# Optimization experiments

Measured on AMD Instinct MI355X. Metric: run time of the kernel, lower is better.

The kernel has to match this reference:

```python
import jax, jax.numpy as jnp
import numpy as np
import math

B, S, DIN, DQ, DV = 8, 2048, 1024, 1024, 1024


def setup_inputs() -> dict:
    key = jax.random.key(0)
    ks = jax.random.split(key, 9)
    c_q = math.sqrt(6.0 / (DIN + DQ))
    c_v = math.sqrt(6.0 / (DIN + DV))
    query = jax.random.normal(ks[0], (B, S, DIN), dtype=jnp.float32)
    key_t = jax.random.normal(ks[1], (B, S, DIN), dtype=jnp.float32)
    value = jax.random.normal(ks[2], (B, S, DIN), dtype=jnp.float32)
    # Linear weights stored as [in, out] for x @ W; uniform init per module
    Wq = jax.random.uniform(ks[3], (DIN, DQ), jnp.float32, -c_q, c_q)
    Wk = jax.random.uniform(ks[4], (DIN, DQ), jnp.float32, -c_q, c_q)
    Wv = jax.random.uniform(ks[5], (DIN, DV), jnp.float32, -c_v, c_v)
    bq = jax.random.uniform(ks[6], (DQ,), jnp.float32, -c_q, c_q)
    bk = jax.random.uniform(ks[7], (DQ,), jnp.float32, -c_q, c_q)
    bv = jax.random.uniform(ks[8], (DV,), jnp.float32, -c_v, c_v)
    # causal mask: True where attention is disallowed (masked_fill semantics)
    mask = jnp.broadcast_to(jnp.triu(jnp.ones((S, S), dtype=bool), k=1), (B, S, S))
    return {"query": query, "key": key_t, "value": value,
            "Wq": Wq, "bq": bq, "Wk": Wk, "bk": bk, "Wv": Wv, "bv": bv,
            "mask": mask}


def reference(query, key, value, Wq, bq, Wk, bk, Wv, bv, mask):
    q = query @ Wq + bq                       # [B,S,DQ]
    k = key @ Wk + bk                         # [B,S,DQ]
    v = value @ Wv + bv                       # [B,S,DV]
    scores = jnp.einsum('bsd,btd->bst', q, k) / math.sqrt(DQ)  # [B,S,S]
    scores = jnp.where(mask, jnp.float32(-1e9), scores)
    weights = jax.nn.softmax(scores, axis=2)
    y = jnp.einsum('bst,btd->bsd', weights, v)  # [B,S,DV]
    return y
```

## Files before the change

### kernel.cpp

```cpp
#include <hip/hip_runtime.h>


typedef unsigned short u16;
typedef unsigned int   u32;
typedef float f32x4 __attribute__((ext_vector_type(4)));
typedef short s16x8 __attribute__((ext_vector_type(8)));

__device__ __forceinline__ u16 f2bf(float x) {
  u32 u = __builtin_bit_cast(u32, x);
  u += 0x7fffu + ((u >> 16) & 1u);
  return (u16)(u >> 16);
}
__device__ __forceinline__ float bf2f(u16 h) {
  u32 u = (u32)h << 16;
  return __builtin_bit_cast(float, u);
}

__device__ __forceinline__ void gld_lds16(const u16* g, u16* l) {
  __builtin_amdgcn_global_load_lds((const __attribute__((address_space(1))) void*)g,
                                   (__attribute__((address_space(3))) void*)l,
                                   16, 0, 0);
}

__global__ __launch_bounds__(256) void cvt_bf16_3(const float* __restrict__ i0,
                                                  const float* __restrict__ i1,
                                                  const float* __restrict__ i2,
                                                  u16* __restrict__ out, long X) {
  const float* in = blockIdx.y == 0 ? i0 : (blockIdx.y == 1 ? i1 : i2);
  long i = (long)blockIdx.x * 256 + threadIdx.x;
  float4 v = ((const float4*)in)[i];
  ushort4 o;
  o.x = f2bf(v.x); o.y = f2bf(v.y); o.z = f2bf(v.z); o.w = f2bf(v.w);
  ((ushort4*)(out + blockIdx.y * X))[i] = o;
}

__global__ __launch_bounds__(256) void transpose_w3(const float* __restrict__ w0,
                                                    const float* __restrict__ w1,
                                                    const float* __restrict__ w2,
                                                    u16* __restrict__ Wt,
                                                    int K, int N, long WN) {
  __shared__ u16 t[32][33];
  const float* W = blockIdx.z == 0 ? w0 : (blockIdx.z == 1 ? w1 : w2);
  u16* out = Wt + blockIdx.z * WN;
  int n0 = blockIdx.x * 32, k0 = blockIdx.y * 32;
  int tx = threadIdx.x & 31, ty = threadIdx.x >> 5;
  for (int r = ty; r < 32; r += 8)
    t[r][tx] = f2bf(W[(long)(k0 + r) * N + n0 + tx]);
  __syncthreads();
  for (int r = ty; r < 32; r += 8)
    out[(long)(n0 + r) * K + k0 + tx] = t[tx][r];
}

__global__ __launch_bounds__(256) void transpose_v(const u16* __restrict__ v,
                                                   u16* __restrict__ vt,
                                                   int S, int D) {
  __shared__ u16 t[32][33];
  long b = blockIdx.z;
  const u16* vb = v + b * S * D;
  u16* vtb = vt + b * S * D;
  int d0 = blockIdx.x * 32, s0 = blockIdx.y * 32;
  int tx = threadIdx.x & 31, ty = threadIdx.x >> 5;
  for (int r = ty; r < 32; r += 8)
    t[r][tx] = vb[(long)(s0 + r) * D + d0 + tx];
  __syncthreads();
  for (int r = ty; r < 32; r += 8)
    vtb[(long)(d0 + r) * S + s0 + tx] = t[tx][r];
}

__device__ __forceinline__ void gemm_core(const u16* __restrict__ At,
                                          const u16* __restrict__ Bt,
                                          int lda, int ldb, int ktEnd,
                                          f32x4 (&acc)[4][4],
                                          u16* lA, u16* lB) {
  const int tid = threadIdx.x;
  const int lane = tid & 63, half = lane >> 4, l16 = lane & 15;
  const int wave = tid >> 6;
  const int wm = (wave >> 1) * 64, wn = (wave & 1) * 64;

  const int c0 = tid, c1 = tid + 256;
  const int r0 = c0 >> 2, kp0 = (c0 & 3) ^ ((c0 >> 3) & 3);
  const int r1 = c1 >> 2, kp1 = (c1 & 3) ^ ((c1 >> 3) & 3);
  const u16* gA0 = At + (long)r0 * lda + kp0 * 8;
  const u16* gA1 = At + (long)r1 * lda + kp1 * 8;
  const u16* gB0 = Bt + (long)r0 * ldb + kp0 * 8;
  const u16* gB1 = Bt + (long)r1 * ldb + kp1 * 8;
  u16* lA0 = lA + c0 * 8; u16* lA1 = lA + c1 * 8;
  u16* lB0 = lB + c0 * 8; u16* lB1 = lB + c1 * 8;
  const int swz = (half ^ ((l16 >> 1) & 3)) * 8;

  for (int kt = 0; kt < ktEnd; ++kt) {
    const int k0 = kt * 32;
    gld_lds16(gA0 + k0, lA0);
    gld_lds16(gA1 + k0, lA1);
    gld_lds16(gB0 + k0, lB0);
    gld_lds16(gB1 + k0, lB1);
    __syncthreads();
    s16x8 af[4], bfr[4];
#pragma unroll
    for (int mi = 0; mi < 4; ++mi)
      af[mi] = *(const s16x8*)&lA[(wm + mi * 16 + l16) * 32 + swz];
#pragma unroll
    for (int ni = 0; ni < 4; ++ni)
      bfr[ni] = *(const s16x8*)&lB[(wn + ni * 16 + l16) * 32 + swz];
#pragma unroll
    for (int mi = 0; mi < 4; ++mi)
#pragma unroll
      for (int ni = 0; ni < 4; ++ni)
        acc[mi][ni] = __builtin_amdgcn_mfma_f32_16x16x32_bf16(af[mi], bfr[ni], acc[mi][ni], 0, 0, 0);
    __syncthreads();
  }
}

struct ProjPtrs {
  const u16* A[3];
  const u16* B[3];
  u16* C[3];
  const float* bias[3];
};

__global__ __launch_bounds__(512, 2)
void gemm_proj(ProjPtrs p) {
  const int H = 32;
  const int f = blockIdx.x;
  const int wg = (f & 7) * 96 + (f >> 3);
  const int bz = wg >> 8;
  const int rr = wg & 255;
  const int bm = rr >> 2, bn = rr & 3;

  __shared__ u16 lds[65536];
  u16* lA = lds;
  u16* lB = lds + 32768;

  const int tid = threadIdx.x;
  const int lane = tid & 63, l16 = lane & 15, lq = lane >> 4;
  const int w = tid >> 6;
  const int wm = (w >> 2) * 128, wn = (w & 3) * 64;

  const u16* At = p.A[bz] + (long)bm * 256 * 1024;
  const u16* Bt = p.B[bz] + (long)bn * 256 * 1024;

  const int srow = tid >> 2;
  const int skp  = (tid & 3) ^ ((tid >> 3) & 3);
  const u16* gA = At + srow * 1024 + skp * 8;
  const u16* gB = Bt + srow * 1024 + skp * 8;
  const int o0 = tid * 8, o1 = tid * 8 + 4096;

  const int fsw = (lq ^ ((l16 >> 1) & 3)) << 3;
  const int aoff = (wm + l16) * 32 + fsw;
  const int boff = (wn + l16) * 32 + fsw;

  f32x4 acc[8][4];
#pragma unroll
  for (int i = 0; i < 8; ++i)
#pragma unroll
    for (int j = 0; j < 4; ++j) { f32x4 z = {0.f, 0.f, 0.f, 0.f}; acc[i][j] = z; }

#define STA(h) { u16* s_ = lA + ((h) & 3) * 8192;                 \
                 gld_lds16(gA + (h) * 32, s_ + o0);               \
                 gld_lds16(gA + (h) * 32 + 128 * 1024, s_ + o1); }
#define STB(h) { u16* s_ = lB + ((h) & 3) * 8192;                 \
                 gld_lds16(gB + (h) * 32, s_ + o0);               \
                 gld_lds16(gB + (h) * 32 + 128 * 1024, s_ + o1); }
#define FENCE asm volatile("" ::: "memory")

  STA(0); STB(0); STA(1); STB(1); STA(2); STB(2);
  asm volatile("s_waitcnt vmcnt(8)" ::: "memory");
  __builtin_amdgcn_s_barrier();
  FENCE;

  for (int t = 0; t < H; ++t) {
    u16* sA = lA + (t & 3) * 8192;
    u16* sB = lB + (t & 3) * 8192;
    s16x8 af[4], bfr[4];
#pragma unroll
    for (int mi = 0; mi < 4; ++mi)
      af[mi] = *(const s16x8*)&sA[aoff + mi * 512];
#pragma unroll
    for (int ni = 0; ni < 4; ++ni)
      bfr[ni] = *(const s16x8*)&sB[boff + ni * 512];
    if (t + 3 < H) STA(t + 3);
    FENCE;
    __builtin_amdgcn_s_barrier();
    asm volatile("s_waitcnt lgkmcnt(0)" ::: "memory");
    __builtin_amdgcn_s_setprio(1);
#pragma unroll
    for (int mi = 0; mi < 4; ++mi)
#pragma unroll
      for (int ni = 0; ni < 4; ++ni)
        acc[mi][ni] = __builtin_amdgcn_mfma_f32_16x16x32_bf16(af[mi], bfr[ni], acc[mi][ni], 0, 0, 0);
    __builtin_amdgcn_s_setprio(0);
    FENCE;
    __builtin_amdgcn_s_barrier();
    FENCE;
#pragma unroll
    for (int mi = 0; mi < 4; ++mi)
      af[mi] = *(const s16x8*)&sA[aoff + 2048 + mi * 512];
    if (t + 3 < H) STB(t + 3);
    FENCE;
    __builtin_amdgcn_s_barrier();
    asm volatile("s_waitcnt lgkmcnt(0)" ::: "memory");
    __builtin_amdgcn_s_setprio(1);
#pragma unroll
    for (int mi = 0; mi < 4; ++mi)
#pragma unroll
      for (int ni = 0; ni < 4; ++ni)
        acc[4 + mi][ni] = __builtin_amdgcn_mfma_f32_16x16x32_bf16(af[mi], bfr[ni], acc[4 + mi][ni], 0, 0, 0);
    __builtin_amdgcn_s_setprio(0);
    if (t < H - 3)       { asm volatile("s_waitcnt vmcnt(8)" ::: "memory"); }
    else if (t == H - 3) { asm volatile("s_waitcnt vmcnt(4)" ::: "memory"); }
    else if (t == H - 2) { asm volatile("s_waitcnt vmcnt(0)" ::: "memory"); }
    FENCE;
    __builtin_amdgcn_s_barrier();
    FENCE;
  }
#undef STA
#undef STB
#undef FENCE

  u16* Cb = p.C[bz];
  const float* bias = p.bias[bz];
  const int colBase = bn * 256 + wn + l16;
  const long rowBase = (long)bm * 256 + wm + lq * 4;
  float bvv[4];
#pragma unroll
  for (int ni = 0; ni < 4; ++ni) bvv[ni] = bias[colBase + ni * 16];
#pragma unroll
  for (int mi = 0; mi < 8; ++mi)
#pragma unroll
    for (int ni = 0; ni < 4; ++ni) {
      const int col = colBase + ni * 16;
#pragma unroll
      for (int r = 0; r < 4; ++r)
        Cb[(rowBase + mi * 16 + r) * 1024 + col] = f2bf(acc[mi][ni][r] + bvv[ni]);
    }
}

__global__ __launch_bounds__(256, 2)
void gemm_scores_exp(const u16* __restrict__ q, const u16* __restrict__ k,
                     u16* __restrict__ E, int ld, long sQK, long sSC,
                     int kTiles, float scale) {
  const int f = blockIdx.x;
  const int bz = f & 7;
  const int t = f >> 3;
  int bm = (int)((sqrtf(8.f * t + 1.f) - 1.f) * 0.5f);
  while ((bm + 1) * (bm + 2) / 2 <= t) ++bm;
  while (bm * (bm + 1) / 2 > t) --bm;
  const int bn = t - bm * (bm + 1) / 2;

  __shared__ u16 lA[128 * 32], lB[128 * 32];
  f32x4 acc[4][4];
#pragma unroll
  for (int i = 0; i < 4; ++i)
#pragma unroll
    for (int j = 0; j < 4; ++j) { f32x4 z = {0.f, 0.f, 0.f, 0.f}; acc[i][j] = z; }

  gemm_core(q + (long)bz * sQK + (long)bm * 128 * ld,
            k + (long)bz * sQK + (long)bn * 128 * ld,
            ld, ld, kTiles, acc, lA, lB);

  const int lane = threadIdx.x & 63, half = lane >> 4, l16 = lane & 15;
  const int wave = threadIdx.x >> 6;
  const int wm = (wave >> 1) * 64, wn = (wave & 1) * 64;
  u16* Eb = E + (long)bz * sSC;
  const int colBase = bn * 128 + wn + l16;
  const int rowBase = bm * 128 + wm + half * 4;
  const bool diag = (bn == bm);
#pragma unroll
  for (int mi = 0; mi < 4; ++mi)
#pragma unroll
    for (int ni = 0; ni < 4; ++ni) {
      int col = colBase + ni * 16;
#pragma unroll
      for (int r = 0; r < 4; ++r) {
        int row = rowBase + mi * 16 + r;
        float e = __expf(acc[mi][ni][r] * scale);
        u16 out = (!diag || col <= row) ? f2bf(e) : (u16)0;
        Eb[(long)row * 2048 + col] = out;
      }
    }
}

__global__ __launch_bounds__(256) void row_inv(const u16* __restrict__ E,
                                               float* __restrict__ inv, int S) {
  const int wave = threadIdx.x >> 6, lane = threadIdx.x & 63;
  const long row = (long)blockIdx.x * 4 + wave;
  const int i = (int)(row & (S - 1));
  const int zend = ((i >> 7) + 1) << 7;
  const u16* erow = E + row * S;
  float s = 0.f;
  for (int c = lane * 4; c < zend; c += 256) {
    ushort4 u = *(const ushort4*)(erow + c);
    s += (bf2f(u.x) + bf2f(u.y)) + (bf2f(u.z) + bf2f(u.w));
  }
  for (int o = 32; o > 0; o >>= 1) s += __shfl_down(s, o);
  if (lane == 0) inv[row] = 1.f / s;
}

__global__ __launch_bounds__(256, 2)
void gemm_pv(const u16* __restrict__ E, const u16* __restrict__ vT,
             const float* __restrict__ inv, float* __restrict__ y,
             int lda, int ldb, int ldc, long sP, long sV, long sY, int S) {
  const int f = blockIdx.x;
  const int bz = f & 7;
  const int g = f >> 3;
  const int bm = 15 - (g >> 3);
  const int bn = g & 7;
  const int ktEnd = (bm + 1) * 4;

  __shared__ u16 lA[128 * 32], lB[128 * 32];
  f32x4 acc[4][4];
#pragma unroll
  for (int i = 0; i < 4; ++i)
#pragma unroll
    for (int j = 0; j < 4; ++j) { f32x4 z = {0.f, 0.f, 0.f, 0.f}; acc[i][j] = z; }

  gemm_core(E + (long)bz * sP + (long)bm * 128 * lda,
            vT + (long)bz * sV + (long)bn * 128 * ldb,
            lda, ldb, ktEnd, acc, lA, lB);

  const int lane = threadIdx.x & 63, half = lane >> 4, l16 = lane & 15;
  const int wave = threadIdx.x >> 6;
  const int wm = (wave >> 1) * 64, wn = (wave & 1) * 64;
  float* Cb = y + (long)bz * sY;
  const float* invb = inv + (long)bz * S;
  const int colBase = bn * 128 + wn + l16;
  const int rowBase = bm * 128 + wm + half * 4;
#pragma unroll
  for (int mi = 0; mi < 4; ++mi) {
    float iv[4];
#pragma unroll
    for (int r = 0; r < 4; ++r) iv[r] = invb[rowBase + mi * 16 + r];
#pragma unroll
    for (int ni = 0; ni < 4; ++ni) {
      int col = colBase + ni * 16;
#pragma unroll
      for (int r = 0; r < 4; ++r)
        Cb[(long)(rowBase + mi * 16 + r) * ldc + col] = acc[mi][ni][r] * iv[r];
    }
  }
}

extern "C" void kernel_launch(void* const* d_in, const int* in_sizes, int n_in,
                              void* d_out, int out_size, void* d_ws, size_t ws_size,
                              hipStream_t stream) {
  const int B = 8, S = 2048, DIN = 1024, DQ = 1024, DV = 1024;
  const long X  = (long)B * S * DIN;
  const long WN = (long)DIN * DQ;

  const float* query = (const float*)d_in[0];
  const float* key   = (const float*)d_in[1];
  const float* value = (const float*)d_in[2];
  const float* Wq = (const float*)d_in[3];
  const float* bq = (const float*)d_in[4];
  const float* Wk = (const float*)d_in[5];
  const float* bk = (const float*)d_in[6];
  const float* Wv = (const float*)d_in[7];
  const float* bv = (const float*)d_in[8];

  u16* w = (u16*)d_ws;
  u16* xq = w;
  u16* WT = w + 3 * X;
  const long R1 = 3 * X + 3 * WN;
  u16* vbuf = w + R1;
  u16* q  = w + R1 + X;
  u16* k  = w + R1 + 2 * X;
  u16* vT = w + R1 + 3 * X;
  u16* E = w;
  float* inv = (float*)(w + 3 * X);

  dim3 blk(256);
  cvt_bf16_3<<<dim3(X / 1024, 3), blk, 0, stream>>>(query, key, value, xq, X);
  transpose_w3<<<dim3(DQ / 32, DIN / 32, 3), blk, 0, stream>>>(Wq, Wk, Wv, WT, DIN, DQ, WN);

  ProjPtrs pp;
  pp.A[0] = xq; pp.A[1] = xq + X; pp.A[2] = xq + 2 * X;
  pp.B[0] = WT; pp.B[1] = WT + WN; pp.B[2] = WT + 2 * WN;
  pp.C[0] = q;  pp.C[1] = k;      pp.C[2] = vbuf;
  pp.bias[0] = bq; pp.bias[1] = bk; pp.bias[2] = bv;
  gemm_proj<<<dim3(768), dim3(512), 0, stream>>>(pp);

  transpose_v<<<dim3(DV / 32, S / 32, B), blk, 0, stream>>>(vbuf, vT, S, DV);

  gemm_scores_exp<<<dim3(136 * 8), blk, 0, stream>>>(
      q, k, E, DQ, X / B, (long)S * S, DQ / 32, 0.03125f);

  row_inv<<<dim3(B * S / 4), blk, 0, stream>>>(E, inv, S);

  gemm_pv<<<dim3(1024), blk, 0, stream>>>(
      E, vT, inv, (float*)d_out, S, S, DV, (long)S * S, (long)DV * S,
      (long)S * DV, S);
}
```

Measured before the change: 572.5 us.

## Double-buffer MFMA fragments in registers and halve barriers per k-step in projection GEMM

Restructures the projection GEMM main loop so that the next k-step's A and B fragments are read from LDS into a second register set while the current MFMAs run. Each k-step now uses one barrier instead of two, and the A and B tile prefetches are issued together. The loop is unrolled by two to swap the B fragment buffers, and the vmcnt waits are retuned for four-load groups. This aims to hide LDS latency and cut synchronisation stalls, at the cost of higher register pressure and an assumption that the k-step count is even.

```diff
diff --git a/kernel.cpp b/kernel.cpp
--- a/kernel.cpp
+++ b/kernel.cpp
@@ -155,6 +155,8 @@
 #pragma unroll
     for (int j = 0; j < 4; ++j) { f32x4 z = {0.f, 0.f, 0.f, 0.f}; acc[i][j] = z; }
 
+  s16x8 af0[4], af1[4], bf0[4], bf1[4];
+
 #define STA(h) { u16* s_ = lA + ((h) & 3) * 8192;                 \
                  gld_lds16(gA + (h) * 32, s_ + o0);               \
                  gld_lds16(gA + (h) * 32 + 128 * 1024, s_ + o1); }
@@ -164,55 +166,58 @@
 #define FENCE asm volatile("" ::: "memory")
 
   STA(0); STB(0); STA(1); STB(1); STA(2); STB(2);
-  asm volatile("s_waitcnt vmcnt(8)" ::: "memory");
+  asm volatile("s_waitcnt vmcnt(4)" ::: "memory");
   __builtin_amdgcn_s_barrier();
   FENCE;
-
-  for (int t = 0; t < H; ++t) {
-    u16* sA = lA + (t & 3) * 8192;
-    u16* sB = lB + (t & 3) * 8192;
-    s16x8 af[4], bfr[4];
-#pragma unroll
-    for (int mi = 0; mi < 4; ++mi)
-      af[mi] = *(const s16x8*)&sA[aoff + mi * 512];
-#pragma unroll
-    for (int ni = 0; ni < 4; ++ni)
-      bfr[ni] = *(const s16x8*)&sB[boff + ni * 512];
-    if (t + 3 < H) STA(t + 3);
-    FENCE;
-    __builtin_amdgcn_s_barrier();
-    asm volatile("s_waitcnt lgkmcnt(0)" ::: "memory");
-    __builtin_amdgcn_s_setprio(1);
-#pragma unroll
-    for (int mi = 0; mi < 4; ++mi)
-#pragma unroll
-      for (int ni = 0; ni < 4; ++ni)
-        acc[mi][ni] = __builtin_amdgcn_mfma_f32_16x16x32_bf16(af[mi], bfr[ni], acc[mi][ni], 0, 0, 0);
-    __builtin_amdgcn_s_setprio(0);
-    FENCE;
-    __builtin_amdgcn_s_barrier();
-    FENCE;
-#pragma unroll
-    for (int mi = 0; mi < 4; ++mi)
-      af[mi] = *(const s16x8*)&sA[aoff + 2048 + mi * 512];
-    if (t + 3 < H) STB(t + 3);
-    FENCE;
-    __builtin_amdgcn_s_barrier();
-    asm volatile("s_waitcnt lgkmcnt(0)" ::: "memory");
-    __builtin_amdgcn_s_setprio(1);
-#pragma unroll
-    for (int mi = 0; mi < 4; ++mi)
-#pragma unroll
-      for (int ni = 0; ni < 4; ++ni)
-        acc[4 + mi][ni] = __builtin_amdgcn_mfma_f32_16x16x32_bf16(af[mi], bfr[ni], acc[4 + mi][ni], 0, 0, 0);
-    __builtin_amdgcn_s_setprio(0);
-    if (t < H - 3)       { asm volatile("s_waitcnt vmcnt(8)" ::: "memory"); }
-    else if (t == H - 3) { asm volatile("s_waitcnt vmcnt(4)" ::: "memory"); }
-    else if (t == H - 2) { asm volatile("s_waitcnt vmcnt(0)" ::: "memory"); }
-    FENCE;
-    __builtin_amdgcn_s_barrier();
-    FENCE;
-  }
+#pragma unroll
+  for (int mi = 0; mi < 4; ++mi)
+    af0[mi] = *(const s16x8*)&lA[aoff + mi * 512];
+#pragma unroll
+  for (int ni = 0; ni < 4; ++ni)
+    bf0[ni] = *(const s16x8*)&lB[boff + ni * 512];
+
+#define KSTEP(t, BCUR, BNXT) {                                              \
+    if ((t) + 3 < H) { STA((t) + 3); STB((t) + 3); }                        \
+    { u16* sT = lA + ((t) & 3) * 8192;                                      \
+      _Pragma("unroll") for (int mi = 0; mi < 4; ++mi)                      \
+        af1[mi] = *(const s16x8*)&sT[aoff + 2048 + mi * 512]; }             \
+    if ((t) + 1 < H) {                                                      \
+      u16* sNB = lB + (((t) + 1) & 3) * 8192;                               \
+      u16* sNA = lA + (((t) + 1) & 3) * 8192;                               \
+      _Pragma("unroll") for (int ni = 0; ni < 4; ++ni)                      \
+        BNXT[ni] = *(const s16x8*)&sNB[boff + ni * 512];                    \
+      _Pragma("unroll") for (int mi = 0; mi < 4; ++mi)                      \
+        af0[mi] = *(const s16x8*)&sNA[aoff + mi * 512];                     \
+    }                                                                       \
+    __builtin_amdgcn_sched_barrier(0);                                      \
+    __builtin_amdgcn_s_setprio(1);                                          \
+    _Pragma("unroll") for (int mi = 0; mi < 4; ++mi)                        \
+      _Pragma("unroll") for (int ni = 0; ni < 4; ++ni)                      \
+        acc[mi][ni] = __builtin_amdgcn_mfma_f32_16x16x32_bf16(af0c[mi], BCUR[ni], acc[mi][ni], 0, 0, 0); \
+    _Pragma("unroll") for (int mi = 0; mi < 4; ++mi)                        \
+      _Pragma("unroll") for (int ni = 0; ni < 4; ++ni)                      \
+        acc[4 + mi][ni] = __builtin_amdgcn_mfma_f32_16x16x32_bf16(af1[mi], BCUR[ni], acc[4 + mi][ni], 0, 0, 0); \
+    __builtin_amdgcn_s_setprio(0);                                          \
+    if ((t) < H - 3)       { asm volatile("s_waitcnt vmcnt(4)" ::: "memory"); } \
+    else if ((t) == H - 3) { asm volatile("s_waitcnt vmcnt(0)" ::: "memory"); } \
+    FENCE;                                                                  \
+    __builtin_amdgcn_s_barrier();                                           \
+    FENCE;                                                                  \
+  }
+
+  for (int t = 0; t < H; t += 2) {
+    {
+      s16x8 af0c[4];
+      _Pragma("unroll") for (int mi = 0; mi < 4; ++mi) af0c[mi] = af0[mi];
+      KSTEP(t, bf0, bf1);
+    }
+    {
+      s16x8 af0c[4];
+      _Pragma("unroll") for (int mi = 0; mi < 4; ++mi) af0c[mi] = af0[mi];
+      KSTEP(t + 1, bf1, bf0);
+    }
+  }
+#undef KSTEP
 #undef STA
 #undef STB
 #undef FENCE
```

Result: no change. 573.6 us (+0.2%).
